# Optimization experiments

Hardware: AMD Instinct MI355X
Metric: run time of the kernel (lower is better)

## Reference

```python
import jax, jax.numpy as jnp
import numpy as np

MIN_LEN = 4      # g.min_word_length
MAX_LEN = 10     # g.max_word_length
THRESH = 0.05    # g.init_threshold
NEG = -1e9


def setup_inputs() -> dict:
    key = jax.random.key(0)
    ks = jax.random.split(key, 6)
    B, L, F, D, U, V = 16, 64, 60, 256, 600, 10000
    x = jax.random.normal(ks[0], (B, L, F), jnp.float32)            # batch dense feat matrix
    unit_feats = jax.random.normal(ks[1], (U, F), jnp.float32)      # per-unit features
    W = jax.random.normal(ks[2], (F, D), jnp.float32) * 0.1         # FeatEmbedding weight
    lengths = jax.random.randint(ks[3], (B,), MIN_LEN, L + 1)       # sentence lengths
    indexed_segments = jax.random.randint(ks[4], (V, MAX_LEN), 0, U)  # vocab -> unit ids
    vocab_length = jax.random.randint(ks[5], (V,), MIN_LEN, MAX_LEN + 1)
    return dict(x=x, unit_feats=unit_feats, W=W, lengths=lengths,
                indexed_segments=indexed_segments, vocab_length=vocab_length)


def reference(x, unit_feats, W, lengths, indexed_segments, vocab_length):
    B, L, _ = x.shape
    V, J = indexed_segments.shape
    # embedding: features -> char_emb space
    word_repr = x @ W                 # [B, L, D]
    unit_repr = unit_feats @ W        # [U, D]
    # cosine similarity between every segment position and every unit
    wn = word_repr / (jnp.linalg.norm(word_repr, axis=-1, keepdims=True) + 1e-8)
    un = unit_repr / (jnp.linalg.norm(unit_repr, axis=-1, keepdims=True) + 1e-8)
    sim = jnp.einsum('bld,ud->blu', wn, un)  # [B, L, U]
    # pad so span gathers past the end read zeros (masked later by `viable`)
    sim_pad = jnp.pad(sim, ((0, 0), (0, J), (0, 0)))
    # accumulate per-position unit scores along each vocab word's unit sequence
    acc = jnp.zeros((B, L, V), sim.dtype)
    per_len = []
    for j in range(J):  # fixed small loop over word-length positions
        # sim at start+j for unit indexed_segments[v, j] -> [B, L, V]
        s_j = sim_pad[:, j:j + L, :][:, :, indexed_segments[:, j]]
        acc = acc + s_j
        if j + 1 >= MIN_LEN:
            per_len.append(acc / (j + 1))  # length-normalized match score
    scores = jnp.stack(per_len, axis=2)  # [B, len_s=L, len_e=E, V]
    E = scores.shape[2]
    k = jnp.arange(E) + MIN_LEN                          # candidate word lengths
    ends = jnp.arange(L)[:, None] + k[None, :] - 1        # [L, E]
    viable = ends[None] < lengths[:, None, None]          # [B, L, E]
    len_match = vocab_length[None, None, None, :] == k[None, None, :, None]
    mask = viable[..., None] & len_match                  # [B, L, E, V]
    masked = jnp.where(mask, scores, NEG)
    # best vocab word per span candidate
    value = masked.max(axis=-1)                           # [B, L, E]
    matched_vocab = masked.argmax(axis=-1)                # [B, L, E]
    matched = value > THRESH
    # best span candidate per batch element (eval path: hard max)
    flat = value.reshape(B, -1)                           # [B, L*E]
    best_inds = flat.argmax(axis=-1)
    best_scores = flat.max(axis=-1)
    best_starts = best_inds // E
    best_ends = best_inds % E + best_starts + MIN_LEN - 1
    any_matched = matched.reshape(B, -1).any(axis=-1)
    best_vocab = jnp.take_along_axis(matched_vocab.reshape(B, -1), best_inds[:, None], axis=1)[:, 0]
    return best_scores, best_starts, best_ends, any_matched, best_vocab
```

## Files before the change

kernel.cpp:

```cpp
#include <hip/hip_runtime.h>
#include <math.h>

#define BB 16
#define LL 64
#define FF 60
#define DD 256
#define UU 600
#define VV 10000
#define JMAX 10
#define MINL 4
#define EE 7
#define NEG (-1e9f)
#define TH 0.05f
#define BCAP 10240

#define UNT_OFF   0
#define WNT_OFF   163840
#define SIM_OFF   425984
#define CNT_OFF   1040384
#define SRT_OFF   1040392
#define VAL_OFF   1613832
#define VOC_OFF   1628168

__global__ __launch_bounds__(256) void k_prep(const int* __restrict__ seg,
                                              const int* __restrict__ vlen,
                                              const float* __restrict__ x,
                                              const float* __restrict__ uf,
                                              const float* __restrict__ W,
                                              unsigned int* __restrict__ cnt,
                                              unsigned int* __restrict__ srt,
                                              float* __restrict__ unT,
                                              float* __restrict__ wnT) {
    int blk = blockIdx.x;
    if (blk < 40) {
        int v = blk * 256 + threadIdx.x;
        if (v >= VV) return;
        int lane = threadIdx.x & 63;
        unsigned long long below = (lane == 0) ? 0ull : (~0ull >> (64 - lane));
        const int* s = seg + v * JMAX;
        unsigned int t[10];
#pragma unroll
        for (int j = 0; j < JMAX; ++j) t[j] = (unsigned int)(s[j] * 11 + j);
        int e = vlen[v] - MINL;
        unsigned int pos = 0;
#pragma unroll
        for (int b2 = 0; b2 < EE; ++b2) {
            unsigned long long m = __ballot(e == b2);
            if (e == b2) {
                int leader = __ffsll((long long)m) - 1;
                unsigned int wc = (unsigned int)__popcll(m);
                unsigned int base = 0;
                if (lane == leader) base = atomicAdd(&cnt[b2], wc);
                base = __shfl(base, leader, 64);
                pos = base + (unsigned int)__popcll(m & below);
            }
        }
        unsigned int* dst = srt + ((size_t)e * BCAP + pos) * 8;
        uint4 qa, qb;
        qa.x = t[0] | (t[1] << 16);
        qa.y = t[2] | (t[3] << 16);
        qa.z = t[4] | (t[5] << 16);
        qa.w = t[6] | (t[7] << 16);
        qb.x = t[8] | (t[9] << 16);
        qb.y = (unsigned int)v;
        qb.z = 0; qb.w = 0;
        ((uint4*)dst)[0] = qa;
        ((uint4*)dst)[1] = qb;
    } else {
        int w = threadIdx.x >> 6;
        int lane = threadIdx.x & 63;
        int id = (blk - 40) * 4 + w;
        const float* row;
        float* outB;
        int stride, col;
        if (id < UU) { row = uf + id * FF; outB = unT; stride = 640;  col = id; }
        else { int bl = id - UU; row = x + bl * FF; outB = wnT; stride = 1024; col = bl; }

        float r0 = 0.f, r1 = 0.f, r2 = 0.f, r3 = 0.f;
#pragma unroll 4
        for (int f = 0; f < FF; ++f) {
            float xv = row[f];
            r0 += xv * W[f * DD + lane];
            r1 += xv * W[f * DD + lane + 64];
            r2 += xv * W[f * DD + lane + 128];
            r3 += xv * W[f * DD + lane + 192];
        }
        float ss = r0 * r0 + r1 * r1 + r2 * r2 + r3 * r3;
#pragma unroll
        for (int m = 32; m > 0; m >>= 1) ss += __shfl_xor(ss, m, 64);
        float inv = 1.0f / (sqrtf(ss) + 1e-8f);
        outB[(lane      ) * stride + col] = r0 * inv;
        outB[(lane +  64) * stride + col] = r1 * inv;
        outB[(lane + 128) * stride + col] = r2 * inv;
        outB[(lane + 192) * stride + col] = r3 * inv;
    }
}

__global__ __launch_bounds__(320) void k_sim(const float* __restrict__ unT,
                                             const float* __restrict__ wnT,
                                             float* __restrict__ sim) {
    int blk = blockIdx.x;
    int b  = blk >> 5;
    int r  = blk & 31;
    int l0 = (r >> 1) * 4;
    int uh = r & 1;
    int bl0 = b * 64 + l0;
    int u = uh * 320 + threadIdx.x;

    float a0 = 0.f, a1 = 0.f, a2 = 0.f, a3 = 0.f;
#pragma unroll 8
    for (int d = 0; d < DD; ++d) {
        float4 wv = *(const float4*)(wnT + d * 1024 + bl0);
        float v  = unT[d * 640 + u];
        a0 += wv.x * v;
        a1 += wv.y * v;
        a2 += wv.z * v;
        a3 += wv.w * v;
    }
    if (u < UU) {
        sim[(bl0 + 0) * UU + u] = a0;
        sim[(bl0 + 1) * UU + u] = a1;
        sim[(bl0 + 2) * UU + u] = a2;
        sim[(bl0 + 3) * UU + u] = a3;
    }
}

template<int K>
__device__ __forceinline__ void bucket_pass(const unsigned int* __restrict__ srt,
                                            const float* __restrict__ lds,
                                            int e, int half, int n, int tid,
                                            float& s0, int& w0,
                                            float& s1, int& w1) {
    int n0 = n >> 1;
    int lo = half ? n0 : 0;
    int hi = half ? n : n0;
    for (int p = lo + tid; p < hi; p += 512) {
        const uint4* pp = (const uint4*)(srt + ((size_t)e * BCAP + p) * 8);
        uint4 qa = pp[0];
        uint4 qb = pp[1];
        unsigned int tw[5] = {qa.x, qa.y, qa.z, qa.w, qb.x};
        int v = (int)qb.y;
        float a0 = 0.f, a1 = 0.f;
#pragma unroll
        for (int j = 0; j < K; ++j) {
            int idx = (int)((tw[j >> 1] >> ((j & 1) * 16)) & 0xffffu);
            float x0 = lds[idx];
            float x1 = lds[idx + 1];
            a0 += x0;
            a1 += x1;
        }
        bool p0 = (a0 > s0) || (a0 == s0 && v < w0);
        bool p1 = (a1 > s1) || (a1 == s1 && v < w1);
        s0 = p0 ? a0 : s0;  w0 = p0 ? v : w0;
        s1 = p1 ? a1 : s1;  w1 = p1 ? v : w1;
    }
}

__global__ __launch_bounds__(512, 8) void k_score(const float* __restrict__ sim,
                                                  const unsigned int* __restrict__ srt,
                                                  const unsigned int* __restrict__ cnt,
                                                  const int* __restrict__ lengths,
                                                  float* __restrict__ val,
                                                  int* __restrict__ voc) {
    __shared__ float lds[UU * 11];
    __shared__ float redS[14][8];
    __shared__ int   redV[14][8];

    int blk = blockIdx.x;
    int half = blk >> 9;
    int rest = blk & 511;
    int b  = rest >> 5;
    int l0 = (rest & 31) * 2;
    int tid = threadIdx.x;

    for (int u = tid; u < UU; u += 512) {
#pragma unroll
        for (int r = 0; r < 11; ++r) {
            int m = l0 + r;
            lds[u * 11 + r] = (m < LL) ? sim[(b * 64 + m) * UU + u] : 0.0f;
        }
    }
    __syncthreads();

    int ne[EE];
#pragma unroll
    for (int e = 0; e < EE; ++e) ne[e] = (int)cnt[e];

    float bS[EE][2];
    int   bV[EE][2];
#pragma unroll
    for (int e = 0; e < EE; ++e) {
        bS[e][0] = -1e30f; bS[e][1] = -1e30f;
        bV[e][0] = VV;     bV[e][1] = VV;
    }

    bucket_pass<4> (srt, lds, 0, half, ne[0], tid, bS[0][0], bV[0][0], bS[0][1], bV[0][1]);
    bucket_pass<5> (srt, lds, 1, half, ne[1], tid, bS[1][0], bV[1][0], bS[1][1], bV[1][1]);
    bucket_pass<6> (srt, lds, 2, half, ne[2], tid, bS[2][0], bV[2][0], bS[2][1], bV[2][1]);
    bucket_pass<7> (srt, lds, 3, half, ne[3], tid, bS[3][0], bV[3][0], bS[3][1], bV[3][1]);
    bucket_pass<8> (srt, lds, 4, half, ne[4], tid, bS[4][0], bV[4][0], bS[4][1], bV[4][1]);
    bucket_pass<9> (srt, lds, 5, half, ne[5], tid, bS[5][0], bV[5][0], bS[5][1], bV[5][1]);
    bucket_pass<10>(srt, lds, 6, half, ne[6], tid, bS[6][0], bV[6][0], bS[6][1], bV[6][1]);

    int w = tid >> 6, lane = tid & 63;
#pragma unroll
    for (int e = 0; e < EE; ++e) {
#pragma unroll
        for (int dl = 0; dl < 2; ++dl) {
            float s = bS[e][dl];
            int vv = bV[e][dl];
#pragma unroll
            for (int off = 32; off > 0; off >>= 1) {
                float os = __shfl_down(s, off, 64);
                int   ov = __shfl_down(vv, off, 64);
                if (os > s || (os == s && ov < vv)) { s = os; vv = ov; }
            }
            if (lane == 0) { redS[e * 2 + dl][w] = s; redV[e * 2 + dl][w] = vv; }
        }
    }
    __syncthreads();

    if (tid < 14) {
        int e  = tid >> 1;
        int dl = tid & 1;
        float s = redS[tid][0];
        int  vv = redV[tid][0];
#pragma unroll
        for (int w2 = 1; w2 < 8; ++w2) {
            float os = redS[tid][w2];
            int   ov = redV[tid][w2];
            if (os > s || (os == s && ov < vv)) { s = os; vv = ov; }
        }
        int lg = l0 + dl;
        int k = e + MINL;
        bool viable = (lg + k - 1) < lengths[b];
        float sn = s / (float)k;
        int o = (half * BB * LL + b * 64 + lg) * EE + e;
        val[o] = viable ? sn : NEG;
        voc[o] = viable ? vv : 0;
    }
}

__global__ __launch_bounds__(512) void k_final(const float* __restrict__ val,
                                               const int* __restrict__ voc,
                                               float* __restrict__ out) {
    __shared__ float sS[8];
    __shared__ int   sI[8];
    __shared__ int   sV[8];
    __shared__ int   sA[8];
    int b = blockIdx.x;
    int t = threadIdx.x;
    float s = -3e38f;
    int idx = 1 << 30;
    int vc = 0;
    int any = 0;
    if (t < LL * EE) {
        int o0 = b * LL * EE + t;
        int o1 = BB * LL * EE + o0;
        float s0 = val[o0], s1 = val[o1];
        int   v0 = voc[o0], v1 = voc[o1];
        bool sel = (s1 > s0) || (s1 == s0 && v1 < v0);
        s  = sel ? s1 : s0;
        vc = sel ? v1 : v0;
        idx = t;
        any = (s > TH) ? 1 : 0;
    }
#pragma unroll
    for (int off = 32; off > 0; off >>= 1) {
        float os = __shfl_down(s, off, 64);
        int   oi = __shfl_down(idx, off, 64);
        int   ov = __shfl_down(vc, off, 64);
        int   oa = __shfl_down(any, off, 64);
        if (os > s || (os == s && oi < idx)) { s = os; idx = oi; vc = ov; }
        any |= oa;
    }
    int w = t >> 6, lane = t & 63;
    if (lane == 0) { sS[w] = s; sI[w] = idx; sV[w] = vc; sA[w] = any; }
    __syncthreads();
    if (t == 0) {
        for (int w2 = 1; w2 < 8; ++w2) {
            float os = sS[w2];
            int   oi = sI[w2];
            if (os > s || (os == s && oi < idx)) { s = os; idx = oi; vc = sV[w2]; }
            any |= sA[w2];
        }
        int start = idx / EE;
        int e = idx - start * EE;
        int end = e + start + MINL - 1;
        out[b]      = s;
        out[16 + b] = (float)start;
        out[32 + b] = (float)end;
        out[48 + b] = any ? 1.0f : 0.0f;
        out[64 + b] = (float)vc;
    }
}

extern "C" void kernel_launch(void* const* d_in, const int* in_sizes, int n_in,
                              void* d_out, int out_size, void* d_ws, size_t ws_size,
                              hipStream_t stream) {
    const float* x       = (const float*)d_in[0];
    const float* uf      = (const float*)d_in[1];
    const float* W       = (const float*)d_in[2];
    const int*   lengths = (const int*)d_in[3];
    const int*   seg     = (const int*)d_in[4];
    const int*   vlen    = (const int*)d_in[5];
    float* out = (float*)d_out;
    float* ws  = (float*)d_ws;

    float*        unT = ws + UNT_OFF;
    float*        wnT = ws + WNT_OFF;
    float*        sim = ws + SIM_OFF;
    unsigned int* cnt = (unsigned int*)(ws + CNT_OFF);
    unsigned int* srt = (unsigned int*)(ws + SRT_OFF);
    float*        val = ws + VAL_OFF;
    int*          voc = (int*)(ws + VOC_OFF);

    hipMemsetAsync(cnt, 0, 8 * sizeof(unsigned int), stream);
    k_prep<<<446, 256, 0, stream>>>(seg, vlen, x, uf, W, cnt, srt, unT, wnT);
    k_sim<<<512, 320, 0, stream>>>(unT, wnT, sim);
    k_score<<<1024, 512, 0, stream>>>(sim, srt, cnt, lengths, val, voc);
    k_final<<<BB, 512, 0, stream>>>(val, voc, out);
}
```

Before: 145.9 us.

## Partition bucket work across waves by weighted cost instead of striding all buckets

Instead of every thread striding through all seven length buckets, each of the 8 waves now gets a contiguous slice of the combined work, weighted by word length. A wave only processes the buckets its slice overlaps, reduces its own partial best in-wave, and writes it to shared memory, which is pre-initialised for buckets it skips. This is meant to cut the per-bucket tail imbalance and the 14 separate end-of-kernel shuffle reductions across all waves. The cost is per-bucket loops with only 64 lanes, which can leave short bucket ranges with idle lanes, plus extra index arithmetic.

```diff
diff --git a/kernel.cpp b/kernel.cpp
--- a/kernel.cpp
+++ b/kernel.cpp
@@ -126,15 +126,13 @@
 }
 
 template<int K>
-__device__ __forceinline__ void bucket_pass(const unsigned int* __restrict__ srt,
-                                            const float* __restrict__ lds,
-                                            int e, int half, int n, int tid,
-                                            float& s0, int& w0,
-                                            float& s1, int& w1) {
-    int n0 = n >> 1;
-    int lo = half ? n0 : 0;
-    int hi = half ? n : n0;
-    for (int p = lo + tid; p < hi; p += 512) {
+__device__ __forceinline__ void seg_pass(const unsigned int* __restrict__ srt,
+                                         const float* __restrict__ lds,
+                                         int e, int r0, int r1, int lane, int wave,
+                                         float (*redS)[8], int (*redV)[8]) {
+    float s0 = -1e30f, s1 = -1e30f;
+    int w0 = VV, w1 = VV;
+    for (int p = r0 + lane; p < r1; p += 64) {
         const uint4* pp = (const uint4*)(srt + ((size_t)e * BCAP + p) * 8);
         uint4 qa = pp[0];
         uint4 qb = pp[1];
@@ -144,15 +142,26 @@
 #pragma unroll
         for (int j = 0; j < K; ++j) {
             int idx = (int)((tw[j >> 1] >> ((j & 1) * 16)) & 0xffffu);
-            float x0 = lds[idx];
-            float x1 = lds[idx + 1];
-            a0 += x0;
-            a1 += x1;
+            a0 += lds[idx];
+            a1 += lds[idx + 1];
         }
         bool p0 = (a0 > s0) || (a0 == s0 && v < w0);
         bool p1 = (a1 > s1) || (a1 == s1 && v < w1);
         s0 = p0 ? a0 : s0;  w0 = p0 ? v : w0;
         s1 = p1 ? a1 : s1;  w1 = p1 ? v : w1;
+    }
+#pragma unroll
+    for (int off = 32; off > 0; off >>= 1) {
+        float os0 = __shfl_down(s0, off, 64);
+        int   ov0 = __shfl_down(w0, off, 64);
+        float os1 = __shfl_down(s1, off, 64);
+        int   ov1 = __shfl_down(w1, off, 64);
+        if (os0 > s0 || (os0 == s0 && ov0 < w0)) { s0 = os0; w0 = ov0; }
+        if (os1 > s1 || (os1 == s1 && ov1 < w1)) { s1 = os1; w1 = ov1; }
+    }
+    if (lane == 0) {
+        redS[e * 2 + 0][wave] = s0; redV[e * 2 + 0][wave] = w0;
+        redS[e * 2 + 1][wave] = s1; redV[e * 2 + 1][wave] = w1;
     }
 }
 
@@ -173,6 +182,10 @@
     int l0 = (rest & 31) * 2;
     int tid = threadIdx.x;
 
+    if (tid < 112) {
+        redS[tid >> 3][tid & 7] = -1e30f;
+        redV[tid >> 3][tid & 7] = VV;
+    }
     for (int u = tid; u < UU; u += 512) {
 #pragma unroll
         for (int r = 0; r < 11; ++r) {
@@ -182,40 +195,41 @@
     }
     __syncthreads();
 
-    int ne[EE];
-#pragma unroll
-    for (int e = 0; e < EE; ++e) ne[e] = (int)cnt[e];
-
-    float bS[EE][2];
-    int   bV[EE][2];
+    int wave = tid >> 6, lane = tid & 63;
+
+    unsigned nlo[EE], nhi[EE], Bw[EE];
+    unsigned Wtot = 0;
 #pragma unroll
     for (int e = 0; e < EE; ++e) {
-        bS[e][0] = -1e30f; bS[e][1] = -1e30f;
-        bV[e][0] = VV;     bV[e][1] = VV;
-    }
-
-    bucket_pass<4> (srt, lds, 0, half, ne[0], tid, bS[0][0], bV[0][0], bS[0][1], bV[0][1]);
-    bucket_pass<5> (srt, lds, 1, half, ne[1], tid, bS[1][0], bV[1][0], bS[1][1], bV[1][1]);
-    bucket_pass<6> (srt, lds, 2, half, ne[2], tid, bS[2][0], bV[2][0], bS[2][1], bV[2][1]);
-    bucket_pass<7> (srt, lds, 3, half, ne[3], tid, bS[3][0], bV[3][0], bS[3][1], bV[3][1]);
-    bucket_pass<8> (srt, lds, 4, half, ne[4], tid, bS[4][0], bV[4][0], bS[4][1], bV[4][1]);
-    bucket_pass<9> (srt, lds, 5, half, ne[5], tid, bS[5][0], bV[5][0], bS[5][1], bV[5][1]);
-    bucket_pass<10>(srt, lds, 6, half, ne[6], tid, bS[6][0], bV[6][0], bS[6][1], bV[6][1]);
-
-    int w = tid >> 6, lane = tid & 63;
+        unsigned n = cnt[e];
+        unsigned lo = half ? (n >> 1) : 0;
+        unsigned hi = half ? n : (n >> 1);
+        nlo[e] = lo; nhi[e] = hi;
+        Bw[e] = Wtot;
+        Wtot += (hi - lo) * (unsigned)(e + MINL);
+    }
+    unsigned qlo = (unsigned)(((unsigned long long)Wtot * (unsigned)wave) >> 3);
+    unsigned qhi = (unsigned)(((unsigned long long)Wtot * (unsigned)(wave + 1)) >> 3);
+
 #pragma unroll
     for (int e = 0; e < EE; ++e) {
-#pragma unroll
-        for (int dl = 0; dl < 2; ++dl) {
-            float s = bS[e][dl];
-            int vv = bV[e][dl];
-#pragma unroll
-            for (int off = 32; off > 0; off >>= 1) {
-                float os = __shfl_down(s, off, 64);
-                int   ov = __shfl_down(vv, off, 64);
-                if (os > s || (os == s && ov < vv)) { s = os; vv = ov; }
-            }
-            if (lane == 0) { redS[e * 2 + dl][w] = s; redV[e * 2 + dl][w] = vv; }
+        unsigned K = (unsigned)(e + MINL);
+        unsigned segw = (nhi[e] - nlo[e]) * K;
+        unsigned Be = Bw[e];
+        if (qhi <= Be || qlo >= Be + segw || segw == 0) continue;
+        unsigned a = (qlo > Be) ? (qlo - Be) : 0;
+        unsigned bb = qhi - Be; if (bb > segw) bb = segw;
+        int r0 = (int)(nlo[e] + (a + K - 1) / K);
+        int r1 = (int)(nlo[e] + (bb + K - 1) / K);
+        if (r1 <= r0) continue;
+        switch (e) {
+            case 0: seg_pass<4> (srt, lds, 0, r0, r1, lane, wave, redS, redV); break;
+            case 1: seg_pass<5> (srt, lds, 1, r0, r1, lane, wave, redS, redV); break;
+            case 2: seg_pass<6> (srt, lds, 2, r0, r1, lane, wave, redS, redV); break;
+            case 3: seg_pass<7> (srt, lds, 3, r0, r1, lane, wave, redS, redV); break;
+            case 4: seg_pass<8> (srt, lds, 4, r0, r1, lane, wave, redS, redV); break;
+            case 5: seg_pass<9> (srt, lds, 5, r0, r1, lane, wave, redS, redV); break;
+            case 6: seg_pass<10>(srt, lds, 6, r0, r1, lane, wave, redS, redV); break;
         }
     }
     __syncthreads();
```

New measurement: 132.8 us. 9.0% less time.
